# Kernel optimization log

Measured on AMD Instinct MI355X. Metric: run time of the kernel, lower is better.

## Reference

```python
import jax, jax.numpy as jnp
import numpy as np

NEG_SLOPE = 0.2
NUM_GRAPHS = 64


def _gatv2_layer(x, src, dst, Wl, bl, Wr, br, att, bias, n_nodes, heads, ch):
    # lin_l (source) and lin_r (target) transforms -> [N, H, C]
    xs = (x @ Wl + bl).reshape(n_nodes, heads, ch)
    xd = (x @ Wr + br).reshape(n_nodes, heads, ch)
    s = xs[src]                                   # [E, H, C] gathered source feats
    e = jax.nn.leaky_relu(s + xd[dst], NEG_SLOPE)  # GATv2: leaky_relu BEFORE att dot
    score = jnp.einsum('ehc,hc->eh', e, att)       # [E, H]
    # segment softmax over edges sharing the same target node
    smax = jax.ops.segment_max(score, dst, num_segments=n_nodes)
    ex = jnp.exp(score - smax[dst])
    denom = jax.ops.segment_sum(ex, dst, num_segments=n_nodes)
    alpha = ex / denom[dst]                        # [E, H]
    out = jax.ops.segment_sum(alpha[:, :, None] * s, dst, num_segments=n_nodes)
    return out.reshape(n_nodes, heads * ch) + bias


def setup_inputs() -> dict:
    key = jax.random.key(0)
    ks = jax.random.split(key, 20)
    N, E, F = 50000, 800000, 128
    H, C = 4, 64
    G = NUM_GRAPHS
    sc = 0.05
    inp = {
        'x': jax.random.normal(ks[0], (N, F), jnp.float32),
        'edge_index': jax.random.randint(ks[1], (2, E), 0, N, jnp.int64 if jax.config.read('jax_enable_x64') else jnp.int32).astype(jnp.int32),
        'batch': jnp.sort(jax.random.randint(ks[2], (N,), 0, G)).astype(jnp.int32),
        'W_l1': jax.random.normal(ks[3], (F, H * C)) * sc,
        'b_l1': jax.random.normal(ks[4], (H * C,)) * sc,
        'W_r1': jax.random.normal(ks[5], (F, H * C)) * sc,
        'b_r1': jax.random.normal(ks[6], (H * C,)) * sc,
        'att1': jax.random.normal(ks[7], (H, C)) * sc,
        'bias1': jax.random.normal(ks[8], (H * C,)) * sc,
        'W_l2': jax.random.normal(ks[9], (H * C, C)) * sc,
        'b_l2': jax.random.normal(ks[10], (C,)) * sc,
        'W_r2': jax.random.normal(ks[11], (H * C, C)) * sc,
        'b_r2': jax.random.normal(ks[12], (C,)) * sc,
        'att2': jax.random.normal(ks[13], (1, C)) * sc,
        'bias2': jax.random.normal(ks[14], (C,)) * sc,
        'W_lin': jax.random.normal(ks[15], (C, 1)) * sc,
        'b_lin': jax.random.normal(ks[16], (1,)) * sc,
    }
    return inp


def reference(x, edge_index, batch, W_l1, b_l1, W_r1, b_r1, att1, bias1,
              W_l2, b_l2, W_r2, b_r2, att2, bias2, W_lin, b_lin):
    N = x.shape[0]
    # PyG GATv2Conv adds self-loops by default
    loops = jnp.arange(N, dtype=edge_index.dtype)
    src = jnp.concatenate([edge_index[0], loops])
    dst = jnp.concatenate([edge_index[1], loops])

    h = _gatv2_layer(x, src, dst, W_l1, b_l1, W_r1, b_r1, att1, bias1, N, 4, 64)
    h = jax.nn.relu(h)  # dropout=identity (eval), norm=Identity
    h = _gatv2_layer(h, src, dst, W_l2, b_l2, W_r2, b_r2, att2, bias2, N, 1, 64)

    # global mean pool over graphs
    sums = jax.ops.segment_sum(h, batch, num_segments=NUM_GRAPHS)
    counts = jax.ops.segment_sum(jnp.ones((N,), h.dtype), batch, num_segments=NUM_GRAPHS)
    pooled = sums / jnp.maximum(counts, 1.0)[:, None]  # [G, 64]
    return pooled @ W_lin + b_lin                      # [G, 1]
```

## Files before the change

kernel.cpp:

```cpp
#include <hip/hip_runtime.h>
#include <hip/hip_bf16.h>
#include <math.h>

typedef __attribute__((ext_vector_type(8))) short short8;
typedef __attribute__((ext_vector_type(4))) float floatx4;
typedef __attribute__((ext_vector_type(4))) int intx4;

#define ATT_SCALE 0.865617024533378f
#define C_ABS 0.6666666666667f
#define PCLAMP 86.5f

__device__ __forceinline__ float bf2f(unsigned short u) {
  union { unsigned int i; float f; } v; v.i = ((unsigned int)u) << 16; return v.f;
}
__device__ __forceinline__ unsigned short f2bf(float f) {
  union { float f; unsigned int u; } v; v.f = f;
  unsigned int r = (v.u + 0x7fffu + ((v.u >> 16) & 1u)) >> 16;
  return (unsigned short)r;
}
__device__ __forceinline__ int imin(int a, int b) { return a < b ? a : b; }
__device__ __forceinline__ int iclamp(int v, int lo, int hi) {
  return v < lo ? lo : (v > hi ? hi : v);
}
__device__ __forceinline__ float uasf(unsigned int u) {
  union { unsigned int i; float f; } v; v.i = u; return v.f;
}
__device__ __forceinline__ float exp2fast(float x) {
#if __has_builtin(__builtin_amdgcn_exp2f)
  return __builtin_amdgcn_exp2f(x);
#else
  return exp2f(x);
#endif
}
__device__ __forceinline__ float sum8(float x) {
  union { float f; int i; } a, t;
  a.f = x;
  t.i = __builtin_amdgcn_update_dpp(0, a.i, 0xB1, 0xF, 0xF, true); a.f += t.f;
  t.i = __builtin_amdgcn_update_dpp(0, a.i, 0x4E, 0xF, 0xF, true); a.f += t.f;
  t.i = __builtin_amdgcn_ds_swizzle(a.i, 0x101F); a.f += t.f;
  return a.f;
}

__global__ void k_sentinel(float* out, float val) {
  if (threadIdx.x < 64) out[threadIdx.x] = val;
}

struct CvtSegs {
  const void* src[10];
  unsigned short* dst[10];
  int len[10];
};

__global__ void k_prep(const void* __restrict__ x, unsigned short* __restrict__ x_c,
                       int n8, CvtSegs segs,
                       const void* __restrict__ s0, const void* __restrict__ s1,
                       const void* __restrict__ s2, const void* __restrict__ s3,
                       unsigned short* __restrict__ d0, unsigned short* __restrict__ d1,
                       unsigned short* __restrict__ d2, unsigned short* __restrict__ d3,
                       const int* __restrict__ edst, int* deg, int E, int N,
                       int* dflag, float* __restrict__ att1s, float* __restrict__ att2s,
                       int nCvt8, int nTransB) {
  __shared__ int csh;
  if (threadIdx.x == 0) csh = 0;
  __syncthreads();
  {
    unsigned short u = ((const unsigned short*)x)[threadIdx.x];
    int e = (u >> 7) & 0xFF;
    atomicAdd(&csh, (u == 0) || (e >= 100 && e <= 145));
  }
  __syncthreads();
  int isf = (csh < 240);

  int b = blockIdx.x;
  if (b < nCvt8) {
    if (!isf) return;
    int i = b * 256 + threadIdx.x;
    if (i >= n8) return;
    const float* s = (const float*)x + (size_t)i * 8;
    ushort4 a, c;
    a.x = f2bf(s[0]); a.y = f2bf(s[1]); a.z = f2bf(s[2]); a.w = f2bf(s[3]);
    c.x = f2bf(s[4]); c.y = f2bf(s[5]); c.z = f2bf(s[6]); c.w = f2bf(s[7]);
    ((ushort4*)x_c)[i * 2] = a;
    ((ushort4*)x_c)[i * 2 + 1] = c;
    return;
  }
  b -= nCvt8;
  if (b < 10) {
    if (b == 0 && threadIdx.x == 0) dflag[0] = isf;
    int i = threadIdx.x;
    if (i < segs.len[b]) {
      float v = isf ? ((const float*)segs.src[b])[i]
                    : bf2f(((const unsigned short*)segs.src[b])[i]);
      segs.dst[b][i] = f2bf(v);
      if (b == 2) att1s[i] = v * ATT_SCALE;
      if (b == 6) att2s[i] = v * ATT_SCALE;
    }
    return;
  }
  b -= 10;
  if (b < nTransB) {
    int idx = b * 256 + threadIdx.x;
    const void* src; unsigned short* dst; int R, C, loc;
    if (idx < 32768)      { src = s0; dst = d0; R = 128; C = 256; loc = idx; }
    else if (idx < 65536) { src = s1; dst = d1; R = 128; C = 256; loc = idx - 32768; }
    else if (idx < 81920) { src = s2; dst = d2; R = 256; C = 64;  loc = idx - 65536; }
    else                  { src = s3; dst = d3; R = 256; C = 64;  loc = idx - 81920; }
    unsigned short u = isf ? f2bf(((const float*)src)[loc])
                           : ((const unsigned short*)src)[loc];
    int r = loc / C, cc = loc - r * C;
    dst[cc * R + r] = u;
    return;
  }
  b -= nTransB;
  int base = b * 1024 + threadIdx.x;
#pragma unroll
  for (int k = 0; k < 4; ++k) {
    int e = base + k * 256;
    if (e < E) atomicAdd(&deg[iclamp(edst[e], 0, N - 1)], 1);
  }
}

__global__ __launch_bounds__(1024) void k_scan1(const int* __restrict__ deg, int* bsum,
                                                int* dhist, int N) {
  __shared__ int sm[1024];
  __shared__ int lh[256];
  int tid = threadIdx.x;
  if (tid < 256) lh[tid] = 0;
  __syncthreads();
  int i = blockIdx.x * 1024 + tid;
  int d = (i < N) ? deg[i] : 0;
  if (i < N) atomicAdd(&lh[imin(d, 255)], 1);
  sm[tid] = (i < N) ? ((d + 4) & ~3) : 0;
  __syncthreads();
  for (int off = 512; off > 0; off >>= 1) {
    if (tid < off) sm[tid] += sm[tid + off];
    __syncthreads();
  }
  if (tid == 0) bsum[blockIdx.x] = sm[0];
  if (tid < 256 && lh[tid]) atomicAdd(&dhist[tid], lh[tid]);
}

__global__ __launch_bounds__(1024) void k_scan3(const int* __restrict__ deg,
                                                const int* __restrict__ bsum,
                                                const int* __restrict__ dhist,
                                                int* dcur,
                                                int* rowptr, int* cursor, int N) {
  __shared__ int sm[1024];
  __shared__ int boff;
  __shared__ int hsc[256];
  int tid = threadIdx.x;
  if (tid == 0) {
    int r = 0;
    for (int b = 0; b < blockIdx.x; ++b) r += bsum[b];
    boff = r;
  }
  int i = blockIdx.x * 1024 + tid;
  int v = (i < N) ? ((deg[i] + 4) & ~3) : 0;
  sm[tid] = v;
  __syncthreads();
  for (int off = 1; off < 1024; off <<= 1) {
    int t = (tid >= off) ? sm[tid - off] : 0;
    __syncthreads();
    sm[tid] += t;
    __syncthreads();
  }
  if (i < N) {
    int ex = sm[tid] - v + boff;
    rowptr[i] = ex;
    cursor[i] = ex;
    if (i == N - 1) rowptr[N] = ex + v;
  }
  int hv = 0;
  if (blockIdx.x == 0 && tid < 256) { hv = dhist[tid]; hsc[tid] = hv; }
  __syncthreads();
  for (int off = 1; off < 256; off <<= 1) {
    int t = 0;
    if (blockIdx.x == 0 && tid < 256 && tid >= off) t = hsc[tid - off];
    __syncthreads();
    if (blockIdx.x == 0 && tid < 256) hsc[tid] += t;
    __syncthreads();
  }
  if (blockIdx.x == 0 && tid < 256) dcur[tid] = hsc[tid] - hv;
}

template <int K, int CT, int RT>
__device__ __forceinline__ void gemm2r_body(
    int bx, int by, int tid,
    const unsigned short* __restrict__ A,
    const unsigned short* __restrict__ BTl, const unsigned short* __restrict__ BTr,
    const unsigned short* __restrict__ bl, const unsigned short* __restrict__ br,
    unsigned short* __restrict__ outl, unsigned short* __restrict__ outr,
    int Nrows, int M) {
  constexpr int KI = K / 32;
  int lane = tid & 63;
  int wave = tid >> 6;
  int r = lane & 15, q = lane >> 4;
  int col0 = by * (4 * CT * 16) + wave * (CT * 16);
  int row0 = bx * (16 * RT);
  short8 Bl[KI][CT], Br[KI][CT];
#pragma unroll
  for (int t = 0; t < CT; ++t) {
    const unsigned short* bpl = BTl + (size_t)(col0 + t * 16 + r) * K + q * 8;
    const unsigned short* bpr = BTr + (size_t)(col0 + t * 16 + r) * K + q * 8;
#pragma unroll
    for (int k = 0; k < KI; ++k) {
      Bl[k][t] = *reinterpret_cast<const short8*>(bpl + k * 32);
      Br[k][t] = *reinterpret_cast<const short8*>(bpr + k * 32);
    }
  }
  float bvl[CT], bvr[CT];
#pragma unroll
  for (int t = 0; t < CT; ++t) {
    bvl[t] = bf2f(bl[col0 + t * 16 + r]);
    bvr[t] = bf2f(br[col0 + t * 16 + r]);
  }
  short8 a[KI], an[KI];
  {
    int ar0 = imin(row0 + r, Nrows - 1);
    const unsigned short* Ap = A + (size_t)ar0 * K + q * 8;
#pragma unroll
    for (int k = 0; k < KI; ++k) a[k] = *reinterpret_cast<const short8*>(Ap + k * 32);
  }
  for (int rt = 0; rt < RT; ++rt) {
    if (rt + 1 < RT) {
      int arn = imin(row0 + (rt + 1) * 16 + r, Nrows - 1);
      const unsigned short* Apn = A + (size_t)arn * K + q * 8;
#pragma unroll
      for (int k = 0; k < KI; ++k) an[k] = *reinterpret_cast<const short8*>(Apn + k * 32);
    }
    floatx4 accl[CT], accr[CT];
#pragma unroll
    for (int t = 0; t < CT; ++t) {
      accl[t] = (floatx4){0.f, 0.f, 0.f, 0.f};
      accr[t] = (floatx4){0.f, 0.f, 0.f, 0.f};
    }
#pragma unroll
    for (int k = 0; k < KI; ++k) {
#pragma unroll
      for (int t = 0; t < CT; ++t) {
        accl[t] = __builtin_amdgcn_mfma_f32_16x16x32_bf16(a[k], Bl[k][t], accl[t], 0, 0, 0);
        accr[t] = __builtin_amdgcn_mfma_f32_16x16x32_bf16(a[k], Br[k][t], accr[t], 0, 0, 0);
      }
    }
#pragma unroll
    for (int t = 0; t < CT; ++t) {
      int col = col0 + t * 16 + r;
#pragma unroll
      for (int rr = 0; rr < 4; ++rr) {
        int row = row0 + rt * 16 + q * 4 + rr;
        if (row < Nrows) {
          outl[(size_t)row * M + col] = f2bf(accl[t][rr] + bvl[t]);
          outr[(size_t)row * M + col] = f2bf(accr[t][rr] + bvr[t]);
        }
      }
    }
#pragma unroll
    for (int k = 0; k < KI; ++k) a[k] = an[k];
  }
}

__global__ __launch_bounds__(256) void k_phase1(
    const unsigned short* __restrict__ A0, const unsigned short* __restrict__ A1,
    const int* __restrict__ dflag,
    const unsigned short* __restrict__ BTl, const unsigned short* __restrict__ BTr,
    const unsigned short* __restrict__ bl, const unsigned short* __restrict__ br,
    unsigned short* __restrict__ outl, unsigned short* __restrict__ outr,
    int Nrows, int M, int nG, int nS,
    const int* __restrict__ esrc, const int* __restrict__ edst,
    const int* __restrict__ rowptr, const int* __restrict__ deg,
    int* cursor, int* colx, int* dcur, int* order, int E, int N) {
  int b = blockIdx.x;
  int m2 = 2 * imin(nG, nS);
  bool isG;
  int idx;
  if (b < m2) { isG = (b & 1) == 0; idx = b >> 1; }
  else        { isG = nG > nS;      idx = imin(nG, nS) + (b - m2); }
  if (isG) {
    const unsigned short* A = dflag[0] ? A1 : A0;
    gemm2r_body<128, 2, 8>(idx >> 1, idx & 1, threadIdx.x, A, BTl, BTr, bl, br,
                           outl, outr, Nrows, M);
    return;
  }
  __shared__ int scnt[256];
  __shared__ int sbase[256];
  int ET = E + N;
  int ETcap = E + 4 * N;
  int base = idx * 1024 + threadIdx.x;
  if (threadIdx.x < 256) scnt[threadIdx.x] = 0;
  __syncthreads();
#pragma unroll
  for (int k = 0; k < 4; ++k) {
    int e = base + k * 256;
    if (e < E) {
      int s = iclamp(esrc[e], 0, N - 1), d = iclamp(edst[e], 0, N - 1);
      int pos = atomicAdd(&cursor[d], 1);
      colx[iclamp(pos, 0, ETcap - 1)] = s;
    }
  }
  bool n0 = false, n1 = false, n2 = false, n3 = false;
  int i0 = 0, i1 = 0, i2 = 0, i3 = 0, b0 = 0, b1 = 0, b2 = 0, b3 = 0;
  int l0 = 0, l1 = 0, l2 = 0, l3 = 0;
#define NODEK(nk, ik, bk, lk, KK) { int e = base + KK * 256;                  \
    if (e >= E && e < ET) { int i = e - E; int bg = rowptr[i]; int dv = deg[i]; \
      colx[bg + dv] = i; int cap = rowptr[i + 1];                             \
      for (int j = bg + dv + 1; j < cap; ++j) colx[j] = 0;                    \
      ik = i; bk = imin(dv, 255); lk = atomicAdd(&scnt[bk], 1); nk = true; } }
  NODEK(n0, i0, b0, l0, 0) NODEK(n1, i1, b1, l1, 1)
  NODEK(n2, i2, b2, l2, 2) NODEK(n3, i3, b3, l3, 3)
#undef NODEK
  __syncthreads();
  if (threadIdx.x < 256 && scnt[threadIdx.x])
    sbase[threadIdx.x] = atomicAdd(&dcur[threadIdx.x], scnt[threadIdx.x]);
  __syncthreads();
  if (n0) order[sbase[b0] + l0] = i0;
  if (n1) order[sbase[b1] + l1] = i1;
  if (n2) order[sbase[b2] + l2] = i2;
  if (n3) order[sbase[b3] + l3] = i3;
}

__global__ __launch_bounds__(256) void k_gemm2r_l2(
    const unsigned short* __restrict__ A,
    const unsigned short* __restrict__ BTl, const unsigned short* __restrict__ BTr,
    const unsigned short* __restrict__ bl, const unsigned short* __restrict__ br,
    unsigned short* __restrict__ outl, unsigned short* __restrict__ outr,
    int Nrows, int M) {
  gemm2r_body<256, 1, 4>(blockIdx.x, 0, threadIdx.x, A, BTl, BTr, bl, br,
                         outl, outr, Nrows, M);
}

#define AGG1(U, KK, REM)                                                     \
  {                                                                          \
    float v0 = uasf(U.x << 16), v1 = uasf(U.x & 0xffff0000u);                \
    float v2 = uasf(U.y << 16), v3 = uasf(U.y & 0xffff0000u);                \
    float v4 = uasf(U.z << 16), v5 = uasf(U.z & 0xffff0000u);                \
    float v6 = uasf(U.w << 16), v7 = uasf(U.w & 0xffff0000u);                \
    float q0 = fmaf(a0, v0, ad0), q1 = fmaf(a1, v1, ad1);                    \
    float q2 = fmaf(a2, v2, ad2), q3 = fmaf(a3, v3, ad3);                    \
    float q4 = fmaf(a4, v4, ad4), q5 = fmaf(a5, v5, ad5);                    \
    float q6 = fmaf(a6, v6, ad6), q7 = fmaf(a7, v7, ad7);                    \
    float p = ((q0 + q1) + (q2 + q3)) + ((q4 + q5) + (q6 + q7));             \
    p = fmaf(c0, fabsf(q0), p); p = fmaf(c1, fabsf(q1), p);                  \
    p = fmaf(c2, fabsf(q2), p); p = fmaf(c3, fabsf(q3), p);                  \
    p = fmaf(c4, fabsf(q4), p); p = fmaf(c5, fabsf(q5), p);                  \
    p = fmaf(c6, fabsf(q6), p); p = fmaf(c7, fabsf(q7), p);                  \
    p = sum8(p);                                                             \
    float lim = (KK < (REM)) ? PCLAMP : -INFINITY;                           \
    p = fminf(p, lim);                                                       \
    float w = exp2fast(p);                                                   \
    l += w;                                                                  \
    o0 = fmaf(w, v0, o0); o1 = fmaf(w, v1, o1);                              \
    o2 = fmaf(w, v2, o2); o3 = fmaf(w, v3, o3);                              \
    o4 = fmaf(w, v4, o4); o5 = fmaf(w, v5, o5);                              \
    o6 = fmaf(w, v6, o6); o7 = fmaf(w, v7, o7);                              \
  }

template <int LOG_ROWB, int LPD_LOG, bool BF16_RELU_OUT>
__device__ __forceinline__ void agg_body(
    const int* __restrict__ rowptr, const int* __restrict__ deg,
    const int* __restrict__ colx, const int* __restrict__ order,
    const unsigned short* __restrict__ xs, const unsigned short* __restrict__ xd,
    const float* __restrict__ atts, const unsigned short* __restrict__ bias,
    void* __restrict__ hout, int N) {
  int lane = threadIdx.x & 63;
  int wid = (blockIdx.x * 256 + threadIdx.x) >> 6;
  constexpr int LPD = 1 << LPD_LOG;
  constexpr int DPW = 64 >> LPD_LOG;
  int g = lane >> LPD_LOG;
  int s = lane & (LPD - 1);
  int di = wid * DPW + g;
  bool valid = di < N;
  int dst = valid ? order[di] : 0;
  int beg = valid ? rowptr[dst] : 0;
  int lenv = valid ? deg[dst] + 1 : 0;
  unsigned int lb = (unsigned int)s * 16;
  int ch0 = s * 8;
  const char* xsb = (const char*)xs;
  floatx4 avl = *(const floatx4*)(atts + ch0);
  floatx4 avh = *(const floatx4*)(atts + ch0 + 4);
  uint4 du = *(const uint4*)((const char*)xd + ((size_t)dst << LOG_ROWB) + lb);
  float a0 = avl[0], a1 = avl[1], a2 = avl[2], a3 = avl[3];
  float a4 = avh[0], a5 = avh[1], a6 = avh[2], a7 = avh[3];
  float d0 = uasf(du.x << 16), d1 = uasf(du.x & 0xffff0000u);
  float d2 = uasf(du.y << 16), d3 = uasf(du.y & 0xffff0000u);
  float d4 = uasf(du.z << 16), d5 = uasf(du.z & 0xffff0000u);
  float d6 = uasf(du.w << 16), d7 = uasf(du.w & 0xffff0000u);
  float ad0 = a0 * d0, ad1 = a1 * d1, ad2 = a2 * d2, ad3 = a3 * d3;
  float ad4 = a4 * d4, ad5 = a5 * d5, ad6 = a6 * d6, ad7 = a7 * d7;
  float c0 = copysignf(C_ABS, a0), c1 = copysignf(C_ABS, a1);
  float c2 = copysignf(C_ABS, a2), c3 = copysignf(C_ABS, a3);
  float c4 = copysignf(C_ABS, a4), c5 = copysignf(C_ABS, a5);
  float c6 = copysignf(C_ABS, a6), c7 = copysignf(C_ABS, a7);
  float l = 0.f;
  float o0 = 0.f, o1 = 0.f, o2 = 0.f, o3 = 0.f;
  float o4 = 0.f, o5 = 0.f, o6 = 0.f, o7 = 0.f;
  const int* cx = colx + beg;
#define GATH(p) (*(const uint4*)(xsb + (((unsigned)(p) << LOG_ROWB) + lb)))
  intx4 qA = *(const intx4*)(cx);
  intx4 qB = *(const intx4*)(cx + 4);
  uint4 uA0 = GATH(qA.x), uA1 = GATH(qA.y), uA2 = GATH(qA.z), uA3 = GATH(qA.w);
  uint4 uB0 = GATH(qB.x), uB1 = GATH(qB.y), uB2 = GATH(qB.z), uB3 = GATH(qB.w);
  for (int e = 0; e < lenv; e += 8) {
    intx4 qC = *(const intx4*)(cx + e + 8);
    intx4 qD = *(const intx4*)(cx + e + 12);
    int rem = lenv - e;
    AGG1(uA0, 0, rem) AGG1(uA1, 1, rem) AGG1(uA2, 2, rem) AGG1(uA3, 3, rem)
    uA0 = GATH(qC.x); uA1 = GATH(qC.y); uA2 = GATH(qC.z); uA3 = GATH(qC.w);
    int rem4 = rem - 4;
    AGG1(uB0, 0, rem4) AGG1(uB1, 1, rem4) AGG1(uB2, 2, rem4) AGG1(uB3, 3, rem4)
    uB0 = GATH(qD.x); uB1 = GATH(qD.y); uB2 = GATH(qD.z); uB3 = GATH(qD.w);
  }
#undef GATH
  if (!valid) return;
  float rl = 1.0f / l;
  uint4 bu = *(const uint4*)((const char*)bias + lb);
  float b0 = uasf(bu.x << 16), b1 = uasf(bu.x & 0xffff0000u);
  float b2 = uasf(bu.y << 16), b3 = uasf(bu.y & 0xffff0000u);
  float b4 = uasf(bu.z << 16), b5 = uasf(bu.z & 0xffff0000u);
  float b6 = uasf(bu.w << 16), b7 = uasf(bu.w & 0xffff0000u);
  float r0 = fmaf(o0, rl, b0), r1 = fmaf(o1, rl, b1);
  float r2 = fmaf(o2, rl, b2), r3 = fmaf(o3, rl, b3);
  float r4 = fmaf(o4, rl, b4), r5 = fmaf(o5, rl, b5);
  float r6 = fmaf(o6, rl, b6), r7 = fmaf(o7, rl, b7);
  if constexpr (BF16_RELU_OUT) {
    r0 = fmaxf(r0, 0.f); r1 = fmaxf(r1, 0.f); r2 = fmaxf(r2, 0.f); r3 = fmaxf(r3, 0.f);
    r4 = fmaxf(r4, 0.f); r5 = fmaxf(r5, 0.f); r6 = fmaxf(r6, 0.f); r7 = fmaxf(r7, 0.f);
    uint4 res;
    res.x = (unsigned)f2bf(r0) | ((unsigned)f2bf(r1) << 16);
    res.y = (unsigned)f2bf(r2) | ((unsigned)f2bf(r3) << 16);
    res.z = (unsigned)f2bf(r4) | ((unsigned)f2bf(r5) << 16);
    res.w = (unsigned)f2bf(r6) | ((unsigned)f2bf(r7) << 16);
    *(uint4*)((char*)hout + ((size_t)dst << LOG_ROWB) + lb) = res;
  } else {
    floatx4 ra = {r0, r1, r2, r3}, rb = {r4, r5, r6, r7};
    char* op = (char*)hout + (size_t)dst * 256 + (unsigned)ch0 * 4;
    *(floatx4*)op = ra;
    *(floatx4*)(op + 16) = rb;
  }
}

__global__ __launch_bounds__(256) void k_agg_h4(
    const int* __restrict__ rowptr, const int* __restrict__ deg,
    const int* __restrict__ colx, const int* __restrict__ order,
    const unsigned short* __restrict__ xs, const unsigned short* __restrict__ xd,
    const float* __restrict__ atts, const unsigned short* __restrict__ bias,
    unsigned short* __restrict__ hout, int N) {
  agg_body<9, 5, true>(rowptr, deg, colx, order, xs, xd, atts, bias, hout, N);
}

__global__ __launch_bounds__(256) void k_agg_h1(
    const int* __restrict__ rowptr, const int* __restrict__ deg,
    const int* __restrict__ colx, const int* __restrict__ order,
    const unsigned short* __restrict__ xs, const unsigned short* __restrict__ xd,
    const float* __restrict__ atts, const unsigned short* __restrict__ bias,
    float* __restrict__ hout, int N) {
  agg_body<7, 3, false>(rowptr, deg, colx, order, xs, xd, atts, bias, hout, N);
}

__global__ __launch_bounds__(256) void k_pool(const float* __restrict__ h2,
                                              const int* __restrict__ batch,
                                              float* pool, int* cnt, int N) {
  int lane = threadIdx.x & 63;
  int wid = (blockIdx.x * 256 + threadIdx.x) >> 6;
  int n0 = wid * 32;
  if (n0 >= N) return;
  int nend = imin(n0 + 32, N);
  float acc = 0.f;
  int c = 0;
  int gcur = iclamp(batch[n0], 0, 63);
  for (int n = n0; n < nend; ++n) {
    int gg = iclamp(batch[n], 0, 63);
    if (gg != gcur) {
      atomicAdd(&pool[gcur * 64 + lane], acc);
      if (lane == 0) atomicAdd(&cnt[gcur], c);
      acc = 0.f; c = 0; gcur = gg;
    }
    acc += h2[(size_t)n * 64 + lane];
    c++;
  }
  atomicAdd(&pool[gcur * 64 + lane], acc);
  if (lane == 0) atomicAdd(&cnt[gcur], c);
}

__global__ void k_final(const float* __restrict__ pool, const int* __restrict__ cnt,
                        const unsigned short* __restrict__ Wlinc,
                        const unsigned short* __restrict__ blinc,
                        float* __restrict__ out) {
  int g = threadIdx.x;
  if (g >= 64) return;
  float inv = 1.f / fmaxf((float)cnt[g], 1.f);
  float s = 0.f;
  for (int c = 0; c < 64; ++c) s += pool[g * 64 + c] * bf2f(Wlinc[c]);
  out[g] = fmaf(s, inv, bf2f(blinc[0]));
}

extern "C" void kernel_launch(void* const* d_in, const int* in_sizes, int n_in,
                              void* d_out, int out_size, void* d_ws, size_t ws_size,
                              hipStream_t stream) {
  const void* x     = d_in[0];
  const int*  ei    = (const int*)d_in[1];
  const int*  batch = (const int*)d_in[2];
  const void* Wl1 = d_in[3];  const void* bl1 = d_in[4];
  const void* Wr1 = d_in[5];  const void* br1 = d_in[6];
  const void* att1 = d_in[7]; const void* bias1 = d_in[8];
  const void* Wl2 = d_in[9];  const void* bl2 = d_in[10];
  const void* Wr2 = d_in[11]; const void* br2 = d_in[12];
  const void* att2 = d_in[13]; const void* bias2 = d_in[14];
  const void* Wlin = d_in[15]; const void* blin = d_in[16];
  float* out = (float*)d_out;

  const int F = 128, HC = 256, C2 = 64;
  int N = in_sizes[0] / F;
  int E = in_sizes[1] / 2;
  int ET = E + N;
  const int* esrc = ei;
  const int* edst = ei + E;

  char* w = (char*)d_ws;
  auto alloc = [&](size_t bytes) {
    char* p = w;
    w += (bytes + 255) & ~(size_t)255;
    return p;
  };
  int* dflag  = (int*)alloc(4);
  int* rowptr = (int*)alloc((size_t)(N + 1) * 4);
  int* cursor = (int*)alloc((size_t)N * 4);
  int* bsum   = (int*)alloc(1024 * 4);
  int* colx   = (int*)alloc((size_t)(E + 4 * N + 1024 + 16) * 4);
  int* order  = (int*)alloc((size_t)N * 4);
  unsigned short* smallc = (unsigned short*)alloc(4096);
  float* att1s = (float*)alloc(256 * 4);
  float* att2s = (float*)alloc(64 * 4);
  unsigned short* Wl1T = (unsigned short*)alloc((size_t)F * HC * 2);
  unsigned short* Wr1T = (unsigned short*)alloc((size_t)F * HC * 2);
  unsigned short* Wl2T = (unsigned short*)alloc((size_t)HC * C2 * 2);
  unsigned short* Wr2T = (unsigned short*)alloc((size_t)HC * C2 * 2);
  int* deg    = (int*)alloc((size_t)N * 4);
  float* pool = (float*)alloc(64 * 64 * 4);
  int* cnt    = (int*)alloc(64 * 4);
  int* dhist  = (int*)alloc(256 * 4);
  int* dcur   = (int*)alloc(256 * 4);
  unsigned short* xs1  = (unsigned short*)alloc((size_t)N * HC * 2);
  unsigned short* xd1  = (unsigned short*)alloc((size_t)N * HC * 2);
  unsigned short* h1   = (unsigned short*)alloc((size_t)N * HC * 2);
  size_t required = (size_t)(w - (char*)d_ws);
  size_t zlen = (size_t)((char*)dcur + 1024 - (char*)deg);

  unsigned short* x_c = h1;
  unsigned short* xs2 = xs1;
  unsigned short* xd2 = xs1 + (size_t)N * C2;
  float*          h2  = (float*)xd1;

  unsigned short* bl1c   = smallc + 0;
  unsigned short* br1c   = smallc + 256;
  unsigned short* att1c  = smallc + 512;
  unsigned short* bias1c = smallc + 768;
  unsigned short* bl2c   = smallc + 1024;
  unsigned short* br2c   = smallc + 1088;
  unsigned short* att2c  = smallc + 1152;
  unsigned short* bias2c = smallc + 1216;
  unsigned short* Wlinc  = smallc + 1280;
  unsigned short* blinc  = smallc + 1344;

  if (ws_size < required) {
    k_sentinel<<<1, 64, 0, stream>>>(out, 1000.f + (float)(ws_size >> 20));
    return;
  }

  hipMemsetAsync(deg, 0, zlen, stream);
  hipMemsetAsync(colx + (size_t)E + N, 0, ((size_t)3 * N + 1024 + 16) * 4, stream);

  CvtSegs segs;
  const void* ssrc[10] = {bl1, br1, att1, bias1, bl2, br2, att2, bias2, Wlin, blin};
  unsigned short* sdst[10] = {bl1c, br1c, att1c, bias1c, bl2c, br2c, att2c, bias2c, Wlinc, blinc};
  int slen[10] = {256, 256, 256, 256, 64, 64, 64, 64, 64, 1};
  for (int i = 0; i < 10; ++i) { segs.src[i] = ssrc[i]; segs.dst[i] = sdst[i]; segs.len[i] = slen[i]; }
  int n8 = N * F / 8;
  int nCvt8 = (n8 + 255) / 256;
  int nTransB = (2 * F * HC + 2 * HC * C2 + 255) / 256;
  int nHist = (E + 1023) / 1024;
  k_prep<<<nCvt8 + 10 + nTransB + nHist, 256, 0, stream>>>(
      x, x_c, n8, segs, Wl1, Wr1, Wl2, Wr2, Wl1T, Wr1T, Wl2T, Wr2T,
      edst, deg, E, N, dflag, att1s, att2s, nCvt8, nTransB);

  int nb = (N + 1023) / 1024;
  k_scan1<<<nb, 1024, 0, stream>>>(deg, bsum, dhist, N);
  k_scan3<<<nb, 1024, 0, stream>>>(deg, bsum, dhist, dcur, rowptr, cursor, N);

  int nG = ((N + 127) / 128) * 2;
  int nS = (ET + 1023) / 1024;
  k_phase1<<<nG + nS, 256, 0, stream>>>(
      (const unsigned short*)x, x_c, dflag, Wl1T, Wr1T, bl1c, br1c, xs1, xd1,
      N, HC, nG, nS, esrc, edst, rowptr, deg, cursor, colx, dcur, order, E, N);

  k_agg_h4<<<(N + 7) / 8, 256, 0, stream>>>(rowptr, deg, colx, order, xs1, xd1,
                                            att1s, bias1c, h1, N);

  k_gemm2r_l2<<<(N + 63) / 64, 256, 0, stream>>>(h1, Wl2T, Wr2T, bl2c, br2c, xs2, xd2, N, C2);
  k_agg_h1<<<(N + 31) / 32, 256, 0, stream>>>(rowptr, deg, colx, order, xs2, xd2,
                                              att2s, bias2c, h2, N);

  int pw = (N + 31) / 32;
  k_pool<<<(pw + 3) / 4, 256, 0, stream>>>(h2, batch, pool, cnt, N);
  k_final<<<1, 64, 0, stream>>>(pool, cnt, Wlinc, blinc, out);
}
```

Before: 345.4 us.

## Fold colx zeroing into prep kernel, reverse agg node order, early-exit gather loop

Moves the memset of the colx padding tail into extra blocks of the prep kernel, removing one launch. The aggregation kernels now walk the degree-sorted order in reverse, so the highest-degree destinations are handled first. The gather loop breaks after each half-chunk once remaining edges run out, which skips the tail's index load and gathers. The 8-lane reduction replaces ds_swizzle with row-broadcast DPP, and the agg grid sizes are recomputed. Reordering may change load balance and cache locality.

```diff
diff --git a/kernel.cpp b/kernel.cpp
--- a/kernel.cpp
+++ b/kernel.cpp
@@ -37,7 +37,9 @@
   a.f = x;
   t.i = __builtin_amdgcn_update_dpp(0, a.i, 0xB1, 0xF, 0xF, true); a.f += t.f;
   t.i = __builtin_amdgcn_update_dpp(0, a.i, 0x4E, 0xF, 0xF, true); a.f += t.f;
-  t.i = __builtin_amdgcn_ds_swizzle(a.i, 0x101F); a.f += t.f;
+  t.i = __builtin_amdgcn_update_dpp(0, a.i, 0x104, 0xF, 0xA, false);
+  t.i = __builtin_amdgcn_update_dpp(t.i, a.i, 0x114, 0xF, 0x5, false);
+  a.f += t.f;
   return a.f;
 }
 
@@ -59,7 +61,8 @@
                        unsigned short* __restrict__ d2, unsigned short* __restrict__ d3,
                        const int* __restrict__ edst, int* deg, int E, int N,
                        int* dflag, float* __restrict__ att1s, float* __restrict__ att2s,
-                       int nCvt8, int nTransB) {
+                       int* __restrict__ colx,
+                       int nCvt8, int nTransB, int nZeroB) {
   __shared__ int csh;
   if (threadIdx.x == 0) csh = 0;
   __syncthreads();
@@ -112,6 +115,17 @@
     return;
   }
   b -= nTransB;
+  if (b < nZeroB) {
+    int lim = (E + N) + 3 * N + 1024 + 16;
+    int base = (E + N) + b * 1024 + threadIdx.x;
+#pragma unroll
+    for (int k = 0; k < 4; ++k) {
+      int j = base + k * 256;
+      if (j < lim) colx[j] = 0;
+    }
+    return;
+  }
+  b -= nZeroB;
   int base = b * 1024 + threadIdx.x;
 #pragma unroll
   for (int k = 0; k < 4; ++k) {
@@ -369,7 +383,7 @@
   int s = lane & (LPD - 1);
   int di = wid * DPW + g;
   bool valid = di < N;
-  int dst = valid ? order[di] : 0;
+  int dst = valid ? order[N - 1 - di] : 0;
   int beg = valid ? rowptr[dst] : 0;
   int lenv = valid ? deg[dst] + 1 : 0;
   unsigned int lb = (unsigned int)s * 16;
@@ -377,19 +391,19 @@
   const char* xsb = (const char*)xs;
   floatx4 avl = *(const floatx4*)(atts + ch0);
   floatx4 avh = *(const floatx4*)(atts + ch0 + 4);
-  uint4 du = *(const uint4*)((const char*)xd + ((size_t)dst << LOG_ROWB) + lb);
   float a0 = avl[0], a1 = avl[1], a2 = avl[2], a3 = avl[3];
   float a4 = avh[0], a5 = avh[1], a6 = avh[2], a7 = avh[3];
+  float c0 = copysignf(C_ABS, a0), c1 = copysignf(C_ABS, a1);
+  float c2 = copysignf(C_ABS, a2), c3 = copysignf(C_ABS, a3);
+  float c4 = copysignf(C_ABS, a4), c5 = copysignf(C_ABS, a5);
+  float c6 = copysignf(C_ABS, a6), c7 = copysignf(C_ABS, a7);
+  uint4 du = *(const uint4*)((const char*)xd + ((size_t)dst << LOG_ROWB) + lb);
   float d0 = uasf(du.x << 16), d1 = uasf(du.x & 0xffff0000u);
   float d2 = uasf(du.y << 16), d3 = uasf(du.y & 0xffff0000u);
   float d4 = uasf(du.z << 16), d5 = uasf(du.z & 0xffff0000u);
   float d6 = uasf(du.w << 16), d7 = uasf(du.w & 0xffff0000u);
   float ad0 = a0 * d0, ad1 = a1 * d1, ad2 = a2 * d2, ad3 = a3 * d3;
   float ad4 = a4 * d4, ad5 = a5 * d5, ad6 = a6 * d6, ad7 = a7 * d7;
-  float c0 = copysignf(C_ABS, a0), c1 = copysignf(C_ABS, a1);
-  float c2 = copysignf(C_ABS, a2), c3 = copysignf(C_ABS, a3);
-  float c4 = copysignf(C_ABS, a4), c5 = copysignf(C_ABS, a5);
-  float c6 = copysignf(C_ABS, a6), c7 = copysignf(C_ABS, a7);
   float l = 0.f;
   float o0 = 0.f, o1 = 0.f, o2 = 0.f, o3 = 0.f;
   float o4 = 0.f, o5 = 0.f, o6 = 0.f, o7 = 0.f;
@@ -399,15 +413,17 @@
   intx4 qB = *(const intx4*)(cx + 4);
   uint4 uA0 = GATH(qA.x), uA1 = GATH(qA.y), uA2 = GATH(qA.z), uA3 = GATH(qA.w);
   uint4 uB0 = GATH(qB.x), uB1 = GATH(qB.y), uB2 = GATH(qB.z), uB3 = GATH(qB.w);
-  for (int e = 0; e < lenv; e += 8) {
+  for (int e = 0;; e += 8) {
     intx4 qC = *(const intx4*)(cx + e + 8);
-    intx4 qD = *(const intx4*)(cx + e + 12);
     int rem = lenv - e;
     AGG1(uA0, 0, rem) AGG1(uA1, 1, rem) AGG1(uA2, 2, rem) AGG1(uA3, 3, rem)
     uA0 = GATH(qC.x); uA1 = GATH(qC.y); uA2 = GATH(qC.z); uA3 = GATH(qC.w);
+    if (rem <= 4) break;
+    intx4 qD = *(const intx4*)(cx + e + 12);
     int rem4 = rem - 4;
     AGG1(uB0, 0, rem4) AGG1(uB1, 1, rem4) AGG1(uB2, 2, rem4) AGG1(uB3, 3, rem4)
     uB0 = GATH(qD.x); uB1 = GATH(qD.y); uB2 = GATH(qD.z); uB3 = GATH(qD.w);
+    if (rem <= 8) break;
   }
 #undef GATH
   if (!valid) return;
@@ -567,7 +583,6 @@
   }
 
   hipMemsetAsync(deg, 0, zlen, stream);
-  hipMemsetAsync(colx + (size_t)E + N, 0, ((size_t)3 * N + 1024 + 16) * 4, stream);
 
   CvtSegs segs;
   const void* ssrc[10] = {bl1, br1, att1, bias1, bl2, br2, att2, bias2, Wlin, blin};
@@ -577,10 +592,11 @@
   int n8 = N * F / 8;
   int nCvt8 = (n8 + 255) / 256;
   int nTransB = (2 * F * HC + 2 * HC * C2 + 255) / 256;
+  int nZeroB = (3 * N + 1024 + 16 + 1023) / 1024;
   int nHist = (E + 1023) / 1024;
-  k_prep<<<nCvt8 + 10 + nTransB + nHist, 256, 0, stream>>>(
+  k_prep<<<nCvt8 + 10 + nTransB + nZeroB + nHist, 256, 0, stream>>>(
       x, x_c, n8, segs, Wl1, Wr1, Wl2, Wr2, Wl1T, Wr1T, Wl2T, Wr2T,
-      edst, deg, E, N, dflag, att1s, att2s, nCvt8, nTransB);
+      edst, deg, E, N, dflag, att1s, att2s, colx, nCvt8, nTransB, nZeroB);
 
   int nb = (N + 1023) / 1024;
   k_scan1<<<nb, 1024, 0, stream>>>(deg, bsum, dhist, N);
@@ -592,11 +608,13 @@
       (const unsigned short*)x, x_c, dflag, Wl1T, Wr1T, bl1c, br1c, xs1, xd1,
       N, HC, nG, nS, esrc, edst, rowptr, deg, cursor, colx, dcur, order, E, N);
 
-  k_agg_h4<<<(N + 7) / 8, 256, 0, stream>>>(rowptr, deg, colx, order, xs1, xd1,
-                                            att1s, bias1c, h1, N);
+  int ng4 = (N + 1) / 2;
+  k_agg_h4<<<(ng4 + 3) / 4, 256, 0, stream>>>(rowptr, deg, colx, order, xs1, xd1,
+                                              att1s, bias1c, h1, N);
 
   k_gemm2r_l2<<<(N + 63) / 64, 256, 0, stream>>>(h1, Wl2T, Wr2T, bl2c, br2c, xs2, xd2, N, C2);
-  k_agg_h1<<<(N + 31) / 32, 256, 0, stream>>>(rowptr, deg, colx, order, xs2, xd2,
+  int ng1 = (N + 7) / 8;
+  k_agg_h1<<<(ng1 + 3) / 4, 256, 0, stream>>>(rowptr, deg, colx, order, xs2, xd2,
                                               att2s, bias2c, h2, N);
 
   int pw = (N + 31) / 32;
```

Measured after the change: 353.3 us. 2.3% more time.
